# Performance work log

Hardware: AMD Instinct MI355X
Metric: run time of the kernel (lower is better)

The kernel has to match this reference:

```python
import jax, jax.numpy as jnp
import numpy as np

B, T, D, U = 64, 512, 256, 512


def setup_inputs() -> dict:
    key = jax.random.key(0)
    ks = jax.random.split(key, 8)
    g = lambda k, shape: (jax.random.normal(k, shape, dtype=jnp.float32) * 0.05)
    return {
        "x": jax.random.normal(ks[0], (B, T, D), dtype=jnp.float32),
        "h0": jnp.zeros((B, U), jnp.float32),
        "c0": jnp.zeros((B, U), jnp.float32),
        "W_f_short": g(ks[1], (D + U, U)),
        "b_f_short": -jnp.ones((U,), jnp.float32),
        "W_f_long": g(ks[2], (D + U, U)),
        "b_f_long": jnp.ones((U,), jnp.float32),
        "W_alpha": g(ks[3], (D + U, U)),
        "b_alpha": jnp.zeros((U,), jnp.float32),
        "W_m": g(ks[4], (D + U, D)),
        "b_m": jnp.zeros((D,), jnp.float32),
        "W_C": g(ks[5], (D + U, U)),
        "b_C": jnp.zeros((U,), jnp.float32),
        "W_o": g(ks[6], (D + U, U)),
        "b_o": jnp.zeros((U,), jnp.float32),
    }


def reference(x, h0, c0, W_f_short, b_f_short, W_f_long, b_f_long,
              W_alpha, b_alpha, W_m, b_m, W_C, b_C, W_o, b_o):
    # Fuse the five matmuls that share the same input hx=[h_prev, x_t]
    # into one; W_C uses a different input (hxm) and stays separate.
    units = h0.shape[-1]
    d = x.shape[-1]
    W_cat = jnp.concatenate([W_f_short, W_f_long, W_alpha, W_o, W_m], axis=1)
    b_cat = jnp.concatenate([b_f_short, b_f_long, b_alpha, b_o, b_m], axis=0)
    splits = np.cumsum([units, units, units, units])[:-0 or None]

    def step(carry, x_t):
        h_prev, c_prev = carry
        hx = jnp.concatenate([h_prev, x_t], axis=-1)          # [B, U+D]
        gates = hx @ W_cat + b_cat                            # [B, 4U+D]
        f_short = jax.nn.sigmoid(gates[:, :units])
        f_long = jax.nn.sigmoid(gates[:, units:2 * units])
        alpha = jax.nn.sigmoid(gates[:, 2 * units:3 * units])
        o_t = jax.nn.sigmoid(gates[:, 3 * units:4 * units])
        m_t = jax.nn.sigmoid(gates[:, 4 * units:])            # [B, D]
        f_t = alpha * f_short + (1.0 - alpha) * f_long
        i_t = 1.0 - f_t
        mod_x = m_t * x_t
        hxm = jnp.concatenate([h_prev, mod_x], axis=-1)
        c_hat = jnp.tanh(hxm @ W_C + b_C)
        c_t = f_t * c_prev + i_t * c_hat
        h_t = o_t * jnp.tanh(c_t)
        return (h_t, c_t), h_t

    xs = jnp.swapaxes(x, 0, 1)                                # [T, B, D]
    (_, _), hs = jax.lax.scan(step, (h0, c0), xs)             # hs: [T, B, U]
    return jnp.swapaxes(hs, 0, 1)                             # [B, T, U]
```

## Files before the change

kernel.cpp:

```cpp
#include <hip/hip_runtime.h>
#include <hip/hip_fp16.h>
#include <math.h>

typedef _Float16 h2 __attribute__((ext_vector_type(2)));
typedef _Float16 h8 __attribute__((ext_vector_type(8)));
typedef float    f4 __attribute__((ext_vector_type(4)));
typedef unsigned short     u16;
typedef unsigned int       u32;
typedef unsigned long long u64;

#define BB 64
#define TT 512
#define DD 256
#define UU 512

#define NBLK 64
#define CPB  44
#define XPB  36
#define UPB  8
#define MPB  4
#define NJ   2816
#define NJX  2304

#define OFF_W1   0ull
#define OFF_W2   (OFF_W1 + 2816ull*512*2)
#define OFF_WX   (OFF_W2 + 512ull*256*2)
#define OFF_B1   (OFF_WX + 2304ull*256*2)
#define OFF_HB   (OFF_B1 + 2816ull*4)
#define OFF_MX   (OFF_HB + 256ull*64*8)
#define OFF_CTR  (OFF_MX + 128ull*64*8)
#define OFF_XPRE (OFF_CTR + 16400ull*4)
#define WS_FULL  (OFF_XPRE + 512ull*2304*64*2)

__device__ __forceinline__ float sigf(float v)     { return 1.0f / (1.0f + __expf(-v)); }
__device__ __forceinline__ float tanhfast(float v) { return 1.0f - 2.0f / (__expf(2.0f * v) + 1.0f); }

__device__ __forceinline__ u64 pack_rec(float a, float b, u32 tag) {
    _Float16 ha = (_Float16)a, hb = (_Float16)b;
    u16 ua, ub;
    __builtin_memcpy(&ua, &ha, 2);
    __builtin_memcpy(&ub, &hb, 2);
    return (u64)((u32)ua | ((u32)ub << 16)) | ((u64)tag << 32);
}

__device__ __forceinline__ int pk5(int g, int u) { return (u >> 3) * 44 + g * 8 + (u & 7); }
__device__ __forceinline__ int pkm(int d)        { return (d >> 2) * 44 + 40 + (d & 3); }

__global__ void repack_kernel(const float* __restrict__ Wfs, const float* __restrict__ Wfl,
                              const float* __restrict__ Wal, const float* __restrict__ Wm,
                              const float* __restrict__ WC,  const float* __restrict__ Wo,
                              const float* __restrict__ bfs, const float* __restrict__ bfl,
                              const float* __restrict__ bal, const float* __restrict__ bm,
                              const float* __restrict__ bC,  const float* __restrict__ bo,
                              const float* __restrict__ h0,
                              _Float16* __restrict__ W1, _Float16* __restrict__ W2,
                              _Float16* __restrict__ WxT, float* __restrict__ b1,
                              u64* __restrict__ hrec, u64* __restrict__ mrec)
{
    const int stride = gridDim.x * blockDim.x;
    const int idx = blockIdx.x * blockDim.x + threadIdx.x;

    for (int i = idx; i < 2816 * 512; i += stride) {
        int J = i >> 9, k = i & 511;
        int blk = J / 44, c = J - blk * 44;
        float v;
        if (c < 40) {
            int grp = c >> 3, u = blk * 8 + (c & 7);
            const float* Wg = (grp == 0) ? Wfs : (grp == 1) ? Wfl : (grp == 2) ? Wal : (grp == 3) ? Wo : WC;
            v = Wg[(size_t)k * 512 + u];
        } else {
            int d = blk * 4 + (c - 40);
            v = Wm[(size_t)k * 256 + d];
        }
        W1[i] = (_Float16)v;
    }
    for (int i = idx; i < 512 * 256; i += stride) {
        int u = i >> 8, dd = i & 255;
        W2[i] = (_Float16)WC[(size_t)(512 + dd) * 512 + u];
    }
    for (int i = idx; i < 2304 * 256; i += stride) {
        int Jx = i >> 8, k2 = i & 255;
        int blk = Jx / 36, lc = Jx - blk * 36;
        float v;
        if (lc < 32) {
            int grp = lc >> 3, u = blk * 8 + (lc & 7);
            const float* Wg = (grp == 0) ? Wfs : (grp == 1) ? Wfl : (grp == 2) ? Wal : Wo;
            v = Wg[(size_t)(512 + k2) * 512 + u];
        } else {
            int d = blk * 4 + (lc - 32);
            v = Wm[(size_t)(512 + k2) * 256 + d];
        }
        WxT[i] = (_Float16)v;
    }
    for (int J = idx; J < 2816; J += stride) {
        int blk = J / 44, c = J - blk * 44;
        float v;
        if (c < 40) {
            int grp = c >> 3, u = blk * 8 + (c & 7);
            v = (grp == 0) ? bfs[u] : (grp == 1) ? bfl[u] : (grp == 2) ? bal[u] : (grp == 3) ? bo[u] : bC[u];
        } else {
            v = bm[blk * 4 + (c - 40)];
        }
        b1[J] = v;
    }
    for (int i = idx; i < 256 * 64; i += stride) {
        int j = i >> 6, b = i & 63;
        float v0 = h0[(size_t)b * UU + 2 * j];
        float v1 = h0[(size_t)b * UU + 2 * j + 1];
        hrec[(size_t)j * 64 + b] = pack_rec(v0, v1, 1u);
    }
    for (int i = idx; i < 128 * 64; i += stride) mrec[i] = 0ull;
}

__global__ __launch_bounds__(256) void xpre_kernel(const float* __restrict__ x,
                                                   const _Float16* __restrict__ WxT,
                                                   _Float16* __restrict__ Xpre)
{
    __shared__ _Float16 As[128 * 32];
    __shared__ _Float16 Bs[128 * 32];

    const int tid  = threadIdx.x;
    const int lane = tid & 63;
    const int w    = tid >> 6;
    const int wm   = w >> 1, wn = w & 1;
    const int quad = lane >> 4, l16 = lane & 15;
    const int row0 = blockIdx.x * 128;
    const int n0   = blockIdx.y * 128;

    f4 acc[4][4];
    for (int i = 0; i < 4; ++i)
        for (int j = 0; j < 4; ++j)
            acc[i][j] = (f4){0.f, 0.f, 0.f, 0.f};

    for (int kt = 0; kt < 8; ++kt) {
        const int k0 = kt * 32;
        {
            int r  = tid >> 3;
            int cg = (tid & 7) * 4;
            for (int rr = r; rr < 128; rr += 32) {
                f4 v = *(const f4*)&x[(size_t)(row0 + rr) * 256 + k0 + cg];
                As[rr * 32 + cg + 0] = (_Float16)v.x;
                As[rr * 32 + cg + 1] = (_Float16)v.y;
                As[rr * 32 + cg + 2] = (_Float16)v.z;
                As[rr * 32 + cg + 3] = (_Float16)v.w;
            }
        }
        {
            int r   = tid & 127;
            int seg = (tid >> 7) * 16;
            const _Float16* src = &WxT[(size_t)(n0 + r) * 256 + k0 + seg];
            *(f4*)&Bs[r * 32 + seg]     = *(const f4*)src;
            *(f4*)&Bs[r * 32 + seg + 8] = *(const f4*)(src + 8);
        }
        __syncthreads();

        h8 af[4], bfr[4];
#pragma unroll
        for (int f = 0; f < 4; ++f) {
            af[f]  = *(const h8*)&As[(wm * 64 + f * 16 + l16) * 32 + quad * 8];
            bfr[f] = *(const h8*)&Bs[(wn * 64 + f * 16 + l16) * 32 + quad * 8];
        }
#pragma unroll
        for (int fm = 0; fm < 4; ++fm)
#pragma unroll
            for (int fn = 0; fn < 4; ++fn)
                acc[fm][fn] = __builtin_amdgcn_mfma_f32_16x16x32_f16(af[fm], bfr[fn], acc[fm][fn], 0, 0, 0);
        __syncthreads();
    }

#pragma unroll
    for (int fm = 0; fm < 4; ++fm)
#pragma unroll
        for (int fn = 0; fn < 4; ++fn)
#pragma unroll
            for (int r = 0; r < 4; ++r) {
                int rr = row0 + wm * 64 + fm * 16 + quad * 4 + r;
                int J  = n0 + wn * 64 + fn * 16 + l16;
                int b = rr >> 9, tt = rr & 511;
                Xpre[((size_t)tt * NJX + J) * 64 + b] = (_Float16)acc[fm][fn][r];
            }
}

__global__ __launch_bounds__(256, 1) void rnn_coop(
    const float* __restrict__ x, const float* __restrict__ c0,
    const _Float16* __restrict__ W1, const _Float16* __restrict__ W2,
    const float* __restrict__ b1, const _Float16* __restrict__ Xpre,
    u64* __restrict__ hrec, u64* __restrict__ mrec,
    float* __restrict__ out)
{
    __shared__ __align__(16) _Float16 sW1[48 * 512];
    __shared__ float sB1[44];

    const int tid  = threadIdx.x;
    const int blk  = blockIdx.x;
    const int lane = tid & 63;
    const int q    = tid >> 6;
    const int l16  = lane & 15;
    const int quad = lane >> 4;
    const int swz  = l16 & 7;
    const int br   = q * 16 + l16;

    for (int idx = tid; idx < 48 * 64; idx += 256) {
        int r = idx >> 6, j = idx & 63;
        h8 v = {};
        if (r < CPB) v = *(const h8*)(W1 + ((size_t)(blk * CPB + r) * 512 + j * 8));
        *(h8*)&sW1[(r * 64 + (j ^ (r & 7))) * 8] = v;
    }
    h8 af2[8];
#pragma unroll
    for (int ks = 0; ks < 8; ++ks) {
        af2[ks] = (h8){};
        if (l16 < 8)
            af2[ks] = *(const h8*)(W2 + (size_t)(blk * UPB + l16) * 256 + ks * 32 + quad * 8);
    }
    if (tid < CPB) sB1[tid] = b1[blk * CPB + tid];
    float cr[4] = {0.f, 0.f, 0.f, 0.f};
    if (quad < 2) {
#pragma unroll
        for (int r = 0; r < 4; ++r)
            cr[r] = c0[(size_t)br * UU + blk * UPB + quad * 4 + r];
    }
    __syncthreads();

    for (int t = 0; t < TT; ++t) {
        const u32 expt = (u32)t + 1u;

        float pfs[4], pflv[4], pal[4], pov[4];
        float pxm[4] = {0.f, 0.f, 0.f, 0.f};
        f4 pxv = {0.f, 0.f, 0.f, 0.f};
        if (quad < 2) {
            const _Float16* xp = Xpre + ((size_t)t * NJX + blk * XPB) * 64 + br;
#pragma unroll
            for (int r = 0; r < 4; ++r) {
                int u = quad * 4 + r;
                pfs[r]  = (float)xp[(size_t)u * 64];
                pflv[r] = (float)xp[(size_t)(8 + u) * 64];
                pal[r]  = (float)xp[(size_t)(16 + u) * 64];
                pov[r]  = (float)xp[(size_t)(24 + u) * 64];
            }
        } else if (quad == 2) {
            const _Float16* xq = Xpre + ((size_t)t * NJX + blk * XPB + 32) * 64 + br;
#pragma unroll
            for (int r = 0; r < 4; ++r) pxm[r] = (float)xq[(size_t)r * 64];
            pxv = *(const f4*)&x[((size_t)br * TT + t) * DD + blk * MPB];
        }

        h8 bf[16];
        {
            u32 guard = 0;
            for (;;) {
                u32 bad = 0;
#pragma unroll
                for (int ks = 0; ks < 16; ++ks) {
                    const int j0 = (ks * 4 + quad) * 4;
                    u64 r0 = __hip_atomic_load(hrec + (size_t)(j0 + 0) * 64 + br,
                                               __ATOMIC_RELAXED, __HIP_MEMORY_SCOPE_AGENT);
                    u64 r1 = __hip_atomic_load(hrec + (size_t)(j0 + 1) * 64 + br,
                                               __ATOMIC_RELAXED, __HIP_MEMORY_SCOPE_AGENT);
                    u64 r2 = __hip_atomic_load(hrec + (size_t)(j0 + 2) * 64 + br,
                                               __ATOMIC_RELAXED, __HIP_MEMORY_SCOPE_AGENT);
                    u64 r3 = __hip_atomic_load(hrec + (size_t)(j0 + 3) * 64 + br,
                                               __ATOMIC_RELAXED, __HIP_MEMORY_SCOPE_AGENT);
                    bad |= ((u32)(r0 >> 32) ^ expt) | ((u32)(r1 >> 32) ^ expt)
                         | ((u32)(r2 >> 32) ^ expt) | ((u32)(r3 >> 32) ^ expt);
                    u32 d[4] = {(u32)r0, (u32)r1, (u32)r2, (u32)r3};
                    __builtin_memcpy(&bf[ks], d, 16);
                }
                if (__all(bad == 0)) break;
                __builtin_amdgcn_s_sleep(2);
                if (++guard > 1000000u) break;
            }
        }

        f4 acc2 = {0.f, 0.f, 0.f, 0.f};
#pragma unroll
        for (int ks = 0; ks < 16; ++ks) {
            int jx = (ks * 4 + quad) ^ swz;
            h8 a2 = *(const h8*)&sW1[((32 + l16) * 64 + jx) * 8];
            acc2 = __builtin_amdgcn_mfma_f32_16x16x32_f16(a2, bf[ks], acc2, 0, 0, 0);
        }
        if (quad == 2) {
            float m0 = sigf(acc2[0] + sB1[40] + pxm[0]) * pxv[0];
            float m1 = sigf(acc2[1] + sB1[41] + pxm[1]) * pxv[1];
            float m2 = sigf(acc2[2] + sB1[42] + pxm[2]) * pxv[2];
            float m3 = sigf(acc2[3] + sB1[43] + pxm[3]) * pxv[3];
            __hip_atomic_store(mrec + (size_t)(blk * 2 + 0) * 64 + br, pack_rec(m0, m1, expt),
                               __ATOMIC_RELAXED, __HIP_MEMORY_SCOPE_AGENT);
            __hip_atomic_store(mrec + (size_t)(blk * 2 + 1) * 64 + br, pack_rec(m2, m3, expt),
                               __ATOMIC_RELAXED, __HIP_MEMORY_SCOPE_AGENT);
        }

        f4 acc0 = {0.f, 0.f, 0.f, 0.f}, acc1 = {0.f, 0.f, 0.f, 0.f};
#pragma unroll
        for (int ks = 0; ks < 16; ++ks) {
            int jx = (ks * 4 + quad) ^ swz;
            h8 a0 = *(const h8*)&sW1[((     l16) * 64 + jx) * 8];
            h8 a1 = *(const h8*)&sW1[((16 + l16) * 64 + jx) * 8];
            acc0 = __builtin_amdgcn_mfma_f32_16x16x32_f16(a0, bf[ks], acc0, 0, 0, 0);
            acc1 = __builtin_amdgcn_mfma_f32_16x16x32_f16(a1, bf[ks], acc1, 0, 0, 0);
        }

        float fv[4], ov[4], cpv[4];
#pragma unroll
        for (int r = 0; r < 4; ++r) {
            float flsh = __shfl_xor(acc0[r], 32);
            float osh  = __shfl_xor(acc1[r], 32);
            if (quad < 2) {
                int u = quad * 4 + r;
                float fs = sigf(acc0[r] + sB1[u]      + pfs[r]);
                float fl = sigf(flsh    + sB1[8 + u]  + pflv[r]);
                float al = sigf(acc1[r] + sB1[16 + u] + pal[r]);
                fv[r]  = al * fs + (1.0f - al) * fl;
                ov[r]  = sigf(osh + sB1[24 + u] + pov[r]);
                cpv[r] = acc2[r] + sB1[32 + u];
            }
        }

        h8 bf2[8];
        {
            u32 guard = 0;
            for (;;) {
                u32 bad = 0;
#pragma unroll
                for (int ks = 0; ks < 8; ++ks) {
                    const int j0 = (ks * 4 + quad) * 4;
                    u64 r0 = __hip_atomic_load(mrec + (size_t)(j0 + 0) * 64 + br,
                                               __ATOMIC_RELAXED, __HIP_MEMORY_SCOPE_AGENT);
                    u64 r1 = __hip_atomic_load(mrec + (size_t)(j0 + 1) * 64 + br,
                                               __ATOMIC_RELAXED, __HIP_MEMORY_SCOPE_AGENT);
                    u64 r2 = __hip_atomic_load(mrec + (size_t)(j0 + 2) * 64 + br,
                                               __ATOMIC_RELAXED, __HIP_MEMORY_SCOPE_AGENT);
                    u64 r3 = __hip_atomic_load(mrec + (size_t)(j0 + 3) * 64 + br,
                                               __ATOMIC_RELAXED, __HIP_MEMORY_SCOPE_AGENT);
                    bad |= ((u32)(r0 >> 32) ^ expt) | ((u32)(r1 >> 32) ^ expt)
                         | ((u32)(r2 >> 32) ^ expt) | ((u32)(r3 >> 32) ^ expt);
                    u32 d[4] = {(u32)r0, (u32)r1, (u32)r2, (u32)r3};
                    __builtin_memcpy(&bf2[ks], d, 16);
                }
                if (__all(bad == 0)) break;
                __builtin_amdgcn_s_sleep(2);
                if (++guard > 1000000u) break;
            }
        }

        f4 aq = {0.f, 0.f, 0.f, 0.f};
#pragma unroll
        for (int ks = 0; ks < 8; ++ks)
            aq = __builtin_amdgcn_mfma_f32_16x16x32_f16(af2[ks], bf2[ks], aq, 0, 0, 0);

        if (quad < 2) {
            float hv[4];
#pragma unroll
            for (int r = 0; r < 4; ++r) {
                float ch = tanhfast(aq[r] + cpv[r]);
                float f  = fv[r];
                float c  = f * cr[r] + (1.0f - f) * ch;
                cr[r] = c;
                hv[r] = ov[r] * tanhfast(c);
            }
            const u32 tagh = (u32)t + 2u;
            const int j0 = blk * 4 + quad * 2;
            __hip_atomic_store(hrec + (size_t)(j0 + 0) * 64 + br, pack_rec(hv[0], hv[1], tagh),
                               __ATOMIC_RELAXED, __HIP_MEMORY_SCOPE_AGENT);
            __hip_atomic_store(hrec + (size_t)(j0 + 1) * 64 + br, pack_rec(hv[2], hv[3], tagh),
                               __ATOMIC_RELAXED, __HIP_MEMORY_SCOPE_AGENT);
            f4 ovec = {hv[0], hv[1], hv[2], hv[3]};
            __builtin_nontemporal_store(ovec,
                (f4*)&out[((size_t)br * TT + t) * UU + blk * UPB + quad * 4]);
        }
    }
}

__global__ __launch_bounds__(704) void rnn_fb(const float* __restrict__ x,
                                              const float* __restrict__ h0,
                                              const float* __restrict__ c0,
                                              const _Float16* __restrict__ W1,
                                              const _Float16* __restrict__ W2,
                                              const _Float16* __restrict__ WxT,
                                              const float* __restrict__ b1g,
                                              float* __restrict__ out)
{
    __shared__ float g_ld[2816];
    __shared__ float b1_ld[2816];
    __shared__ float h_ld[512];
    __shared__ float x_ld[256];
    __shared__ float f_ld[512];
    __shared__ float o_ld[512];
    __shared__ float c_ld[512];
    __shared__ __align__(16) h2 hx_h2[256];
    __shared__ __align__(16) h2 x16_h2[128];
    __shared__ __align__(16) h2 modx_h2[128];

    const int tid = threadIdx.x;
    const int b   = blockIdx.x;
    const int j0  = tid * 4;
    const int c   = j0 % 44;
    const bool hasx = (c < 32) || (c >= 40);
    const int Jx0 = (j0 / 44) * 36 + (c < 32 ? c : c - 8);

    for (int j = tid; j < 2816; j += 704) b1_ld[j] = b1g[j];
    if (tid < 512) {
        h_ld[tid] = h0[b * 512 + tid];
        c_ld[tid] = c0[b * 512 + tid];
    }
    __syncthreads();

    const f4* __restrict__ w1r = (const f4*)(W1 + (size_t)j0 * 512);
    const float* __restrict__ xrow = x + (size_t)b * TT * DD;
    float* __restrict__ orow = out + (size_t)b * TT * UU;

    for (int t = 0; t < TT; ++t) {
        if (tid < 256) {
            h2 p; p[0] = (_Float16)h_ld[2 * tid]; p[1] = (_Float16)h_ld[2 * tid + 1];
            hx_h2[tid] = p;
        } else if (tid < 384) {
            int i = tid - 256;
            float v0 = xrow[t * DD + 2 * i];
            float v1 = xrow[t * DD + 2 * i + 1];
            x_ld[2 * i] = v0; x_ld[2 * i + 1] = v1;
            h2 p; p[0] = (_Float16)v0; p[1] = (_Float16)v1;
            x16_h2[i] = p;
        }
        __syncthreads();

        float a0 = b1_ld[j0], a1 = b1_ld[j0 + 1], a2 = b1_ld[j0 + 2], a3 = b1_ld[j0 + 3];
        if (hasx) {
            const f4* xr0 = (const f4*)(WxT + (size_t)Jx0 * 256);
            const f4* xr1 = xr0 + 32;
            const f4* xr2 = xr0 + 64;
            const f4* xr3 = xr0 + 96;
            const f4* xv4 = (const f4*)x16_h2;
#pragma unroll 4
            for (int kc = 0; kc < 32; ++kc) {
                f4 xv = xv4[kc];
                f4 w0 = xr0[kc], w1 = xr1[kc], w2 = xr2[kc], w3 = xr3[kc];
                const h2* xpv = (const h2*)&xv;
                const h2* p0 = (const h2*)&w0; const h2* p1 = (const h2*)&w1;
                const h2* p2 = (const h2*)&w2; const h2* p3 = (const h2*)&w3;
#pragma unroll
                for (int u = 0; u < 4; ++u) {
                    a0 = __builtin_amdgcn_fdot2(p0[u], xpv[u], a0, false);
                    a1 = __builtin_amdgcn_fdot2(p1[u], xpv[u], a1, false);
                    a2 = __builtin_amdgcn_fdot2(p2[u], xpv[u], a2, false);
                    a3 = __builtin_amdgcn_fdot2(p3[u], xpv[u], a3, false);
                }
            }
        }
        {
            const f4* hx4 = (const f4*)hx_h2;
            const f4* r0 = w1r;
            const f4* r1 = w1r + 64;
            const f4* r2 = w1r + 128;
            const f4* r3 = w1r + 192;
#pragma unroll 4
            for (int kc = 0; kc < 64; ++kc) {
                f4 hv = hx4[kc];
                f4 w0 = r0[kc], w1 = r1[kc], w2 = r2[kc], w3 = r3[kc];
                const h2* hp = (const h2*)&hv;
                const h2* p0 = (const h2*)&w0; const h2* p1 = (const h2*)&w1;
                const h2* p2 = (const h2*)&w2; const h2* p3 = (const h2*)&w3;
#pragma unroll
                for (int u = 0; u < 4; ++u) {
                    a0 = __builtin_amdgcn_fdot2(p0[u], hp[u], a0, false);
                    a1 = __builtin_amdgcn_fdot2(p1[u], hp[u], a1, false);
                    a2 = __builtin_amdgcn_fdot2(p2[u], hp[u], a2, false);
                    a3 = __builtin_amdgcn_fdot2(p3[u], hp[u], a3, false);
                }
            }
        }
        g_ld[j0] = a0; g_ld[j0 + 1] = a1; g_ld[j0 + 2] = a2; g_ld[j0 + 3] = a3;
        __syncthreads();

        if (tid < 128) {
            float m0 = sigf(g_ld[pkm(2 * tid)]);
            float m1 = sigf(g_ld[pkm(2 * tid + 1)]);
            h2 p;
            p[0] = (_Float16)(m0 * x_ld[2 * tid]);
            p[1] = (_Float16)(m1 * x_ld[2 * tid + 1]);
            modx_h2[tid] = p;
        } else if (tid < 640) {
            int u = tid - 128;
            float fs = sigf(g_ld[pk5(0, u)]);
            float fl = sigf(g_ld[pk5(1, u)]);
            float al = sigf(g_ld[pk5(2, u)]);
            f_ld[u] = al * fs + (1.0f - al) * fl;
            o_ld[u] = sigf(g_ld[pk5(3, u)]);
        }
        __syncthreads();

        if (tid < 512) {
            float s = g_ld[pk5(4, tid)];
            const f4* w2r = (const f4*)(W2 + (size_t)tid * 256);
            const f4* mx4 = (const f4*)modx_h2;
#pragma unroll 4
            for (int kc = 0; kc < 32; ++kc) {
                f4 wv = w2r[kc];
                f4 mv = mx4[kc];
                const h2* wp = (const h2*)&wv;
                const h2* mp = (const h2*)&mv;
#pragma unroll
                for (int u = 0; u < 4; ++u)
                    s = __builtin_amdgcn_fdot2(wp[u], mp[u], s, false);
            }
            float ch = tanhfast(s);
            float f  = f_ld[tid];
            float cc = f * c_ld[tid] + (1.0f - f) * ch;
            c_ld[tid] = cc;
            float h  = o_ld[tid] * tanhfast(cc);
            h_ld[tid] = h;
            orow[t * UU + tid] = h;
        }
        __syncthreads();
    }
}

extern "C" void kernel_launch(void* const* d_in, const int* in_sizes, int n_in,
                              void* d_out, int out_size, void* d_ws, size_t ws_size,
                              hipStream_t stream)
{
    (void)in_sizes; (void)n_in; (void)out_size;
    const float* x   = (const float*)d_in[0];
    const float* h0  = (const float*)d_in[1];
    const float* c0  = (const float*)d_in[2];
    const float* Wfs = (const float*)d_in[3];
    const float* bfs = (const float*)d_in[4];
    const float* Wfl = (const float*)d_in[5];
    const float* bfl = (const float*)d_in[6];
    const float* Wal = (const float*)d_in[7];
    const float* bal = (const float*)d_in[8];
    const float* Wm  = (const float*)d_in[9];
    const float* bm  = (const float*)d_in[10];
    const float* WC  = (const float*)d_in[11];
    const float* bC  = (const float*)d_in[12];
    const float* Wo  = (const float*)d_in[13];
    const float* bo  = (const float*)d_in[14];

    char* ws = (char*)d_ws;
    _Float16* W1   = (_Float16*)(ws + OFF_W1);
    _Float16* W2   = (_Float16*)(ws + OFF_W2);
    _Float16* WxT  = (_Float16*)(ws + OFF_WX);
    float*    b1   = (float*)   (ws + OFF_B1);
    u64*      hrec = (u64*)     (ws + OFF_HB);
    u64*      mrec = (u64*)     (ws + OFF_MX);
    _Float16* Xpre = (_Float16*)(ws + OFF_XPRE);

    repack_kernel<<<dim3(1024), dim3(256), 0, stream>>>(
        Wfs, Wfl, Wal, Wm, WC, Wo, bfs, bfl, bal, bm, bC, bo, h0,
        W1, W2, WxT, b1, hrec, mrec);

    if (ws_size >= WS_FULL) {
        xpre_kernel<<<dim3(256, 18), dim3(256), 0, stream>>>(x, WxT, Xpre);
        rnn_coop<<<dim3(NBLK), dim3(256), 0, stream>>>(
            x, c0, W1, W2, b1, Xpre, hrec, mrec, (float*)d_out);
    } else {
        rnn_fb<<<dim3(BB), dim3(704), 0, stream>>>(
            x, h0, c0, W1, W2, WxT, b1, (float*)d_out);
    }
}
```

Measured before the change: 4.055 ms.

## Speculatively prefetch h/m records and poll sentinel words instead of full gathers

In the persistent recurrent kernel, the h-record gather for the next step is issued right after publishing h, and the m-record loads are issued before the f/o MFMAs so their latency overlaps compute. On a tag mismatch, each lane spins on a single sentinel record before redoing the full gather, which cuts polling traffic. MFMA sections are also wrapped in s_setprio to favour compute waves. The cost is extra register pressure from holding the prefetched records, plus more complex wait logic whose sentinel choice must match the writer order.

```diff
diff --git a/kernel.cpp b/kernel.cpp
--- a/kernel.cpp
+++ b/kernel.cpp
@@ -41,6 +41,55 @@
     __builtin_memcpy(&ua, &ha, 2);
     __builtin_memcpy(&ub, &hb, 2);
     return (u64)((u32)ua | ((u32)ub << 16)) | ((u64)tag << 32);
+}
+
+__device__ __forceinline__ u32 gather_h(const u64* __restrict__ hrec, int br, int quad,
+                                        u32 expt, h8 bf[16]) {
+    u32 bad = 0;
+#pragma unroll
+    for (int ks = 0; ks < 16; ++ks) {
+        const int j0 = (ks * 4 + quad) * 4;
+        u64 r0 = __hip_atomic_load(hrec + (size_t)(j0 + 0) * 64 + br,
+                                   __ATOMIC_RELAXED, __HIP_MEMORY_SCOPE_AGENT);
+        u64 r1 = __hip_atomic_load(hrec + (size_t)(j0 + 1) * 64 + br,
+                                   __ATOMIC_RELAXED, __HIP_MEMORY_SCOPE_AGENT);
+        u64 r2 = __hip_atomic_load(hrec + (size_t)(j0 + 2) * 64 + br,
+                                   __ATOMIC_RELAXED, __HIP_MEMORY_SCOPE_AGENT);
+        u64 r3 = __hip_atomic_load(hrec + (size_t)(j0 + 3) * 64 + br,
+                                   __ATOMIC_RELAXED, __HIP_MEMORY_SCOPE_AGENT);
+        bad |= ((u32)(r0 >> 32) ^ expt) | ((u32)(r1 >> 32) ^ expt)
+             | ((u32)(r2 >> 32) ^ expt) | ((u32)(r3 >> 32) ^ expt);
+        u32 d[4] = {(u32)r0, (u32)r1, (u32)r2, (u32)r3};
+        __builtin_memcpy(&bf[ks], d, 16);
+    }
+    return bad;
+}
+
+__device__ __forceinline__ void issue_mx(const u64* __restrict__ mrec, int br, int quad,
+                                         u64 mr[8][4]) {
+#pragma unroll
+    for (int ks = 0; ks < 8; ++ks) {
+        const int j0 = (ks * 4 + quad) * 4;
+#pragma unroll
+        for (int j = 0; j < 4; ++j)
+            mr[ks][j] = __hip_atomic_load(mrec + (size_t)(j0 + j) * 64 + br,
+                                          __ATOMIC_RELAXED, __HIP_MEMORY_SCOPE_AGENT);
+    }
+}
+
+__device__ __forceinline__ u32 check_mx(const u64 mr[8][4], u32 expt, h8 bf2[8]) {
+    u32 bad = 0;
+#pragma unroll
+    for (int ks = 0; ks < 8; ++ks) {
+        u32 d[4];
+#pragma unroll
+        for (int j = 0; j < 4; ++j) {
+            bad |= ((u32)(mr[ks][j] >> 32)) ^ expt;
+            d[j] = (u32)mr[ks][j];
+        }
+        __builtin_memcpy(&bf2[ks], d, 16);
+    }
+    return bad;
 }
 
 __device__ __forceinline__ int pk5(int g, int u) { return (u >> 3) * 44 + g * 8 + (u & 7); }
@@ -222,6 +271,12 @@
     }
     __syncthreads();
 
+    const u64* hsent = hrec + (size_t)(lane * 4 + 3) * 64 + (q * 16 + (lane & 15));
+    const u64* msent = mrec + (size_t)(lane * 2 + 1) * 64 + (q * 16 + (lane & 15));
+
+    h8 bf[16];
+    u32 badh = gather_h(hrec, br, quad, 1u, bf);
+
     for (int t = 0; t < TT; ++t) {
         const u32 expt = (u32)t + 1u;
 
@@ -245,40 +300,29 @@
             pxv = *(const f4*)&x[((size_t)br * TT + t) * DD + blk * MPB];
         }
 
-        h8 bf[16];
         {
             u32 guard = 0;
-            for (;;) {
-                u32 bad = 0;
-#pragma unroll
-                for (int ks = 0; ks < 16; ++ks) {
-                    const int j0 = (ks * 4 + quad) * 4;
-                    u64 r0 = __hip_atomic_load(hrec + (size_t)(j0 + 0) * 64 + br,
-                                               __ATOMIC_RELAXED, __HIP_MEMORY_SCOPE_AGENT);
-                    u64 r1 = __hip_atomic_load(hrec + (size_t)(j0 + 1) * 64 + br,
-                                               __ATOMIC_RELAXED, __HIP_MEMORY_SCOPE_AGENT);
-                    u64 r2 = __hip_atomic_load(hrec + (size_t)(j0 + 2) * 64 + br,
-                                               __ATOMIC_RELAXED, __HIP_MEMORY_SCOPE_AGENT);
-                    u64 r3 = __hip_atomic_load(hrec + (size_t)(j0 + 3) * 64 + br,
-                                               __ATOMIC_RELAXED, __HIP_MEMORY_SCOPE_AGENT);
-                    bad |= ((u32)(r0 >> 32) ^ expt) | ((u32)(r1 >> 32) ^ expt)
-                         | ((u32)(r2 >> 32) ^ expt) | ((u32)(r3 >> 32) ^ expt);
-                    u32 d[4] = {(u32)r0, (u32)r1, (u32)r2, (u32)r3};
-                    __builtin_memcpy(&bf[ks], d, 16);
+            while (!__all(badh == 0)) {
+                for (;;) {
+                    u64 s = __hip_atomic_load(hsent, __ATOMIC_RELAXED, __HIP_MEMORY_SCOPE_AGENT);
+                    if (__all((u32)(s >> 32) == expt)) break;
+                    __builtin_amdgcn_s_sleep(2);
+                    if (++guard > 2000000u) break;
                 }
-                if (__all(bad == 0)) break;
-                __builtin_amdgcn_s_sleep(2);
-                if (++guard > 1000000u) break;
+                badh = gather_h(hrec, br, quad, expt, bf);
+                if (guard > 2000000u) break;
             }
         }
 
         f4 acc2 = {0.f, 0.f, 0.f, 0.f};
+        __builtin_amdgcn_s_setprio(1);
 #pragma unroll
         for (int ks = 0; ks < 16; ++ks) {
             int jx = (ks * 4 + quad) ^ swz;
             h8 a2 = *(const h8*)&sW1[((32 + l16) * 64 + jx) * 8];
             acc2 = __builtin_amdgcn_mfma_f32_16x16x32_f16(a2, bf[ks], acc2, 0, 0, 0);
         }
+        __builtin_amdgcn_s_setprio(0);
         if (quad == 2) {
             float m0 = sigf(acc2[0] + sB1[40] + pxm[0]) * pxv[0];
             float m1 = sigf(acc2[1] + sB1[41] + pxm[1]) * pxv[1];
@@ -290,7 +334,11 @@
                                __ATOMIC_RELAXED, __HIP_MEMORY_SCOPE_AGENT);
         }
 
+        u64 mr[8][4];
+        issue_mx(mrec, br, quad, mr);
+
         f4 acc0 = {0.f, 0.f, 0.f, 0.f}, acc1 = {0.f, 0.f, 0.f, 0.f};
+        __builtin_amdgcn_s_setprio(1);
 #pragma unroll
         for (int ks = 0; ks < 16; ++ks) {
             int jx = (ks * 4 + quad) ^ swz;
@@ -299,6 +347,7 @@
             acc0 = __builtin_amdgcn_mfma_f32_16x16x32_f16(a0, bf[ks], acc0, 0, 0, 0);
             acc1 = __builtin_amdgcn_mfma_f32_16x16x32_f16(a1, bf[ks], acc1, 0, 0, 0);
         }
+        __builtin_amdgcn_s_setprio(0);
 
         float fv[4], ov[4], cpv[4];
 #pragma unroll
@@ -317,36 +366,28 @@
         }
 
         h8 bf2[8];
+        u32 badm = check_mx(mr, expt, bf2);
         {
             u32 guard = 0;
-            for (;;) {
-                u32 bad = 0;
-#pragma unroll
-                for (int ks = 0; ks < 8; ++ks) {
-                    const int j0 = (ks * 4 + quad) * 4;
-                    u64 r0 = __hip_atomic_load(mrec + (size_t)(j0 + 0) * 64 + br,
-                                               __ATOMIC_RELAXED, __HIP_MEMORY_SCOPE_AGENT);
-                    u64 r1 = __hip_atomic_load(mrec + (size_t)(j0 + 1) * 64 + br,
-                                               __ATOMIC_RELAXED, __HIP_MEMORY_SCOPE_AGENT);
-                    u64 r2 = __hip_atomic_load(mrec + (size_t)(j0 + 2) * 64 + br,
-                                               __ATOMIC_RELAXED, __HIP_MEMORY_SCOPE_AGENT);
-                    u64 r3 = __hip_atomic_load(mrec + (size_t)(j0 + 3) * 64 + br,
-                                               __ATOMIC_RELAXED, __HIP_MEMORY_SCOPE_AGENT);
-                    bad |= ((u32)(r0 >> 32) ^ expt) | ((u32)(r1 >> 32) ^ expt)
-                         | ((u32)(r2 >> 32) ^ expt) | ((u32)(r3 >> 32) ^ expt);
-                    u32 d[4] = {(u32)r0, (u32)r1, (u32)r2, (u32)r3};
-                    __builtin_memcpy(&bf2[ks], d, 16);
+            while (!__all(badm == 0)) {
+                for (;;) {
+                    u64 s = __hip_atomic_load(msent, __ATOMIC_RELAXED, __HIP_MEMORY_SCOPE_AGENT);
+                    if (__all((u32)(s >> 32) == expt)) break;
+                    __builtin_amdgcn_s_sleep(2);
+                    if (++guard > 2000000u) break;
                 }
-                if (__all(bad == 0)) break;
-                __builtin_amdgcn_s_sleep(2);
-                if (++guard > 1000000u) break;
+                issue_mx(mrec, br, quad, mr);
+                badm = check_mx(mr, expt, bf2);
+                if (guard > 2000000u) break;
             }
         }
 
         f4 aq = {0.f, 0.f, 0.f, 0.f};
+        __builtin_amdgcn_s_setprio(1);
 #pragma unroll
         for (int ks = 0; ks < 8; ++ks)
             aq = __builtin_amdgcn_mfma_f32_16x16x32_f16(af2[ks], bf2[ks], aq, 0, 0, 0);
+        __builtin_amdgcn_s_setprio(0);
 
         if (quad < 2) {
             float hv[4];
@@ -368,6 +409,9 @@
             __builtin_nontemporal_store(ovec,
                 (f4*)&out[((size_t)br * TT + t) * UU + blk * UPB + quad * 4]);
         }
+
+        if (t + 1 < TT)
+            badh = gather_h(hrec, br, quad, (u32)t + 2u, bf);
     }
 }
 
```

Measured after the change: 9.706 ms. 2.39x slower.
